# Performance work log

Measured on AMD Instinct MI355X. Metric: run time of the kernel, lower is better.

Reference implementation:

```python
import jax, jax.numpy as jnp
import numpy as np

LEAK_RATE = 0.2
SPECTRAL_RADIUS = 0.9


def setup_inputs() -> dict:
    key = jax.random.key(0)
    k1, k2, k3 = jax.random.split(key, 3)
    B, T, D, U = 32, 1024, 256, 1024
    # glorot-uniform-like init
    lim_w = np.sqrt(6.0 / (U + U)).astype(np.float32)
    lim_in = np.sqrt(6.0 / (D + U)).astype(np.float32)
    W = jax.random.uniform(k1, (U, U), jnp.float32, -lim_w, lim_w)
    # rescale reservoir to target spectral radius (done once at build, like the tf layer)
    eig = np.linalg.eigvals(np.asarray(W))
    W = W * (SPECTRAL_RADIUS / np.max(np.abs(eig)).astype(np.float32))
    W_in = jax.random.uniform(k2, (D, U), jnp.float32, -lim_in, lim_in)
    x = jax.random.normal(k3, (B, T, D), jnp.float32)
    return {"x": x, "W": W, "W_in": W_in}


def reference(x, W, W_in):
    # x: [B, T, D] -> outputs [B, T, U]
    B = x.shape[0]
    U = W.shape[0]
    # precompute input projection for all timesteps: [B, T, U]
    xin = jnp.einsum('btd,du->btu', x, W_in)
    xin_t = jnp.swapaxes(xin, 0, 1)  # [T, B, U]

    def step(h, u_t):
        h_new = (1.0 - LEAK_RATE) * h + LEAK_RATE * jnp.tanh(u_t + h @ W)
        return h_new, h_new

    h0 = jnp.zeros((B, U), x.dtype)
    _, ys = jax.lax.scan(step, h0, xin_t)  # ys: [T, B, U]
    return jnp.swapaxes(ys, 0, 1)  # [B, T, U]
```

## Files before the change

kernel.cpp:

```cpp
#include <hip/hip_runtime.h>
#include <stdint.h>


#define T_   1024
#define D_   256
#define U_   1024
#define NTHR 512
#define HROW 1040
#define BAIL (1u << 20)

typedef _Float16     f16x8 __attribute__((ext_vector_type(8)));
typedef float        f32x4 __attribute__((ext_vector_type(4)));
typedef unsigned int u32x4 __attribute__((ext_vector_type(4)));

#if defined(__has_builtin) && __has_builtin(__builtin_amdgcn_rcpf)
__device__ __forceinline__ float rcp_fast(float v) { return __builtin_amdgcn_rcpf(v); }
#else
__device__ __forceinline__ float rcp_fast(float v) { return 1.f / v; }
#endif

__device__ __forceinline__ float tanh_fast(float v) {
    float e = __expf(2.f * v);
    return 1.f - 2.f * rcp_fast(e + 1.f);
}

__device__ __forceinline__ unsigned f2u16(_Float16 v) {
    return (unsigned)__builtin_bit_cast(unsigned short, v);
}

__device__ __forceinline__ void lds_barrier() {
    asm volatile("s_waitcnt lgkmcnt(0)" ::: "memory");
    __builtin_amdgcn_sched_barrier(0);
    __builtin_amdgcn_s_barrier();
}

__device__ __forceinline__ void lds_fence() {
    asm volatile("s_waitcnt lgkmcnt(0)" ::: "memory");
    __builtin_amdgcn_sched_barrier(0);
}

__global__ __launch_bounds__(NTHR, 2) void k_recur(const float* __restrict__ x,
                                                   const float* __restrict__ W,
                                                   const float* __restrict__ win,
                                                   float* __restrict__ out,
                                                   u32x4* __restrict__ hc) {
    __shared__ short hl16[4 * HROW];
    __shared__ f32x4 part4[256];
    unsigned int* hl32 = (unsigned int*)hl16;

    const int tid  = threadIdx.x;
    const int dom  = blockIdx.x & 7;
    const int wg   = blockIdx.x >> 3;
    const int c0   = wg * 32;
    const int b0   = dom * 4;
    const int lane = tid & 63;
    const int wv   = tid >> 6;
    const int l15  = lane & 15;
    const int lg   = lane >> 4;

    f16x8 bw[5][2];
#pragma unroll
    for (int kt = 0; kt < 4; ++kt)
#pragma unroll
        for (int ct = 0; ct < 2; ++ct)
#pragma unroll
            for (int j = 0; j < 8; ++j)
                bw[kt][ct][j] =
                    (_Float16)W[(size_t)(wv * 128 + kt * 32 + lg * 8 + j) * U_ + c0 + ct * 16 + l15];
#pragma unroll
    for (int ct = 0; ct < 2; ++ct)
#pragma unroll
        for (int j = 0; j < 8; ++j)
            bw[4][ct][j] =
                (_Float16)win[(size_t)(wv * 32 + lg * 8 + j) * U_ + c0 + ct * 16 + l15];

    for (int i = tid; i < 2 * HROW; i += NTHR) hl32[i] = 0;
    __syncthreads();

    const int ab = (l15 & 3) * HROW + lg * 8;
    const float* xg = &x[((size_t)(b0 + (l15 & 3)) * T_) * D_ + wv * 32 + lg * 8];

    float4 xa = *(const float4*)xg;
    float4 xc = *(const float4*)(xg + 4);
    xg += D_;

    float hs0 = 0.f, hs1 = 0.f, hs2 = 0.f, hs3 = 0.f;

    for (int t = 0; t < T_; ++t) {
        u32x4 va, vb;
        if (t > 0) {
            const u32x4* pp = hc + (size_t)((t & 1) * 8192 + dom * 1024 + 2 * tid);
            unsigned spin = 0;
            int ok;
            for (;;) {
                asm volatile(
                    "global_load_dwordx4 %0, %2, off sc1\n\t"
                    "global_load_dwordx4 %1, %2, off offset:16 sc1\n\t"
                    "s_waitcnt vmcnt(0)"
                    : "=&v"(va), "=&v"(vb)
                    : "v"(pp) : "memory");
                unsigned tg = (unsigned)t;
                ok = ((va[0] & 0xffffu) == tg) & ((va[1] & 0xffffu) == tg) &
                     ((va[2] & 0xffffu) == tg) & ((va[3] & 0xffffu) == tg) &
                     ((vb[0] & 0xffffu) == tg) & ((vb[1] & 0xffffu) == tg) &
                     ((vb[2] & 0xffffu) == tg) & ((vb[3] & 0xffffu) == tg);
                if (__all(ok) || ++spin > BAIL) break;
                __builtin_amdgcn_s_sleep(1);
            }
#pragma unroll
            for (int b = 0; b < 4; ++b)
                hl32[b * (HROW / 2) + tid] = (va[b] >> 16) | (vb[b] & 0xffff0000u);
        }

        f16x8 xf;
        xf[0] = (_Float16)xa.x; xf[1] = (_Float16)xa.y;
        xf[2] = (_Float16)xa.z; xf[3] = (_Float16)xa.w;
        xf[4] = (_Float16)xc.x; xf[5] = (_Float16)xc.y;
        xf[6] = (_Float16)xc.z; xf[7] = (_Float16)xc.w;

        lds_fence();

        if (t + 1 < T_) {
            xa = *(const float4*)xg;
            xc = *(const float4*)(xg + 4);
            xg += D_;
        }

        f32x4 acc0 = {0.f, 0.f, 0.f, 0.f}, acc1 = {0.f, 0.f, 0.f, 0.f};
#pragma unroll
        for (int kt = 0; kt < 4; ++kt) {
            f16x8 av = *reinterpret_cast<const f16x8*>(&hl16[ab + wv * 128 + kt * 32]);
            acc0 = __builtin_amdgcn_mfma_f32_16x16x32_f16(av, bw[kt][0], acc0, 0, 0, 0);
            acc1 = __builtin_amdgcn_mfma_f32_16x16x32_f16(av, bw[kt][1], acc1, 0, 0, 0);
        }
        acc0 = __builtin_amdgcn_mfma_f32_16x16x32_f16(xf, bw[4][0], acc0, 0, 0, 0);
        acc1 = __builtin_amdgcn_mfma_f32_16x16x32_f16(xf, bw[4][1], acc1, 0, 0, 0);

        if (lane < 16) {
            part4[wv * 32 + l15]      = acc0;
            part4[wv * 32 + 16 + l15] = acc1;
        }
        lds_barrier();

        if (tid < 32) {
            f32x4 s = part4[tid];
#pragma unroll
            for (int w2 = 1; w2 < 8; ++w2) s += part4[w2 * 32 + tid];
            float h0 = 0.8f * hs0 + 0.2f * tanh_fast(s[0]);
            float h1 = 0.8f * hs1 + 0.2f * tanh_fast(s[1]);
            float h2 = 0.8f * hs2 + 0.2f * tanh_fast(s[2]);
            float h3 = 0.8f * hs3 + 0.2f * tanh_fast(s[3]);
            hs0 = h0; hs1 = h1; hs2 = h2; hs3 = h3;
            unsigned tg = (unsigned)(t + 1) & 0xffffu;
            unsigned p0 = (f2u16((_Float16)h0) << 16) | tg;
            unsigned p1 = (f2u16((_Float16)h1) << 16) | tg;
            unsigned p2 = (f2u16((_Float16)h2) << 16) | tg;
            unsigned p3 = (f2u16((_Float16)h3) << 16) | tg;
            unsigned long long q0 = (unsigned long long)p0 | ((unsigned long long)p1 << 32);
            unsigned long long q1 = (unsigned long long)p2 | ((unsigned long long)p3 << 32);
            unsigned long long* dst = (unsigned long long*)
                (hc + (size_t)((((t + 1) & 1) * 8192) + dom * 1024 + c0 + tid));
            __hip_atomic_store(&dst[0], q0, __ATOMIC_RELAXED, __HIP_MEMORY_SCOPE_AGENT);
            __hip_atomic_store(&dst[1], q1, __ATOMIC_RELAXED, __HIP_MEMORY_SCOPE_AGENT);
            size_t ob = ((size_t)b0 * T_ + t) * U_ + c0 + tid;
            out[ob]                       = h0;
            out[ob + (size_t)T_ * U_]     = h1;
            out[ob + (size_t)2 * T_ * U_] = h2;
            out[ob + (size_t)3 * T_ * U_] = h3;
        }
        lds_barrier();
    }
}

extern "C" void kernel_launch(void* const* d_in, const int* in_sizes, int n_in,
                              void* d_out, int out_size, void* d_ws, size_t ws_size,
                              hipStream_t stream) {
    const float* x   = (const float*)d_in[0];
    const float* W   = (const float*)d_in[1];
    const float* win = (const float*)d_in[2];
    float* out = (float*)d_out;

    u32x4* hc = (u32x4*)d_ws;
    if (ws_size < 2 * 8 * 1024 * 16) return;

    hipMemsetAsync(d_ws, 0, 2 * 8 * 1024 * 16, stream);
    k_recur<<<dim3(256), dim3(NTHR), 0, stream>>>(x, W, win, out, hc);
}
```

Baseline: 1.429 ms.

## Double-buffer partial sums and spread the epilogue across all waves

The partial-sum LDS buffer is double-buffered by timestep parity, which lets the second block barrier per step go away. The reduction, tanh, publish and output store are now spread over 16 lanes in each of the 8 waves, each handling one (column, batch) element, instead of 32 threads in one wave handling four batches each. This shortens the serial critical path of each recurrent step. The cost is a larger LDS footprint and more, smaller scattered global stores per step.

```diff
diff --git a/kernel.cpp b/kernel.cpp
--- a/kernel.cpp
+++ b/kernel.cpp
@@ -45,8 +45,10 @@
                                                    float* __restrict__ out,
                                                    u32x4* __restrict__ hc) {
     __shared__ short hl16[4 * HROW];
-    __shared__ f32x4 part4[256];
-    unsigned int* hl32 = (unsigned int*)hl16;
+    __shared__ f32x4 part4[2][256];
+    unsigned int* hl32  = (unsigned int*)hl16;
+    float*        partf = (float*)part4;
+    unsigned int* hc32  = (unsigned int*)hc;
 
     const int tid  = threadIdx.x;
     const int dom  = blockIdx.x & 7;
@@ -84,7 +86,9 @@
     float4 xc = *(const float4*)(xg + 4);
     xg += D_;
 
-    float hs0 = 0.f, hs1 = 0.f, hs2 = 0.f, hs3 = 0.f;
+    const int fcol = wv * 4 + (l15 >> 2);
+    const int fbat = lane & 3;
+    float hs = 0.f;
 
     for (int t = 0; t < T_; ++t) {
         u32x4 va, vb;
@@ -137,38 +141,24 @@
         acc1 = __builtin_amdgcn_mfma_f32_16x16x32_f16(xf, bw[4][1], acc1, 0, 0, 0);
 
         if (lane < 16) {
-            part4[wv * 32 + l15]      = acc0;
-            part4[wv * 32 + 16 + l15] = acc1;
+            part4[t & 1][wv * 32 + l15]      = acc0;
+            part4[t & 1][wv * 32 + 16 + l15] = acc1;
         }
         lds_barrier();
 
-        if (tid < 32) {
-            f32x4 s = part4[tid];
+        if (lane < 16) {
+            float s = 0.f;
 #pragma unroll
-            for (int w2 = 1; w2 < 8; ++w2) s += part4[w2 * 32 + tid];
-            float h0 = 0.8f * hs0 + 0.2f * tanh_fast(s[0]);
-            float h1 = 0.8f * hs1 + 0.2f * tanh_fast(s[1]);
-            float h2 = 0.8f * hs2 + 0.2f * tanh_fast(s[2]);
-            float h3 = 0.8f * hs3 + 0.2f * tanh_fast(s[3]);
-            hs0 = h0; hs1 = h1; hs2 = h2; hs3 = h3;
-            unsigned tg = (unsigned)(t + 1) & 0xffffu;
-            unsigned p0 = (f2u16((_Float16)h0) << 16) | tg;
-            unsigned p1 = (f2u16((_Float16)h1) << 16) | tg;
-            unsigned p2 = (f2u16((_Float16)h2) << 16) | tg;
-            unsigned p3 = (f2u16((_Float16)h3) << 16) | tg;
-            unsigned long long q0 = (unsigned long long)p0 | ((unsigned long long)p1 << 32);
-            unsigned long long q1 = (unsigned long long)p2 | ((unsigned long long)p3 << 32);
-            unsigned long long* dst = (unsigned long long*)
-                (hc + (size_t)((((t + 1) & 1) * 8192) + dom * 1024 + c0 + tid));
-            __hip_atomic_store(&dst[0], q0, __ATOMIC_RELAXED, __HIP_MEMORY_SCOPE_AGENT);
-            __hip_atomic_store(&dst[1], q1, __ATOMIC_RELAXED, __HIP_MEMORY_SCOPE_AGENT);
-            size_t ob = ((size_t)b0 * T_ + t) * U_ + c0 + tid;
-            out[ob]                       = h0;
-            out[ob + (size_t)T_ * U_]     = h1;
-            out[ob + (size_t)2 * T_ * U_] = h2;
-            out[ob + (size_t)3 * T_ * U_] = h3;
+            for (int w2 = 0; w2 < 8; ++w2)
+                s += partf[(t & 1) * 1024 + (w2 * 32 + fcol) * 4 + fbat];
+            float hn = 0.8f * hs + 0.2f * tanh_fast(s);
+            hs = hn;
+            unsigned pk = (f2u16((_Float16)hn) << 16) | ((unsigned)(t + 1) & 0xffffu);
+            __hip_atomic_store(
+                &hc32[(size_t)(((t + 1) & 1) * 32768 + dom * 4096 + (c0 + fcol) * 4 + fbat)],
+                pk, __ATOMIC_RELAXED, __HIP_MEMORY_SCOPE_AGENT);
+            out[((size_t)(b0 + fbat) * T_ + t) * U_ + c0 + fcol] = hn;
         }
-        lds_barrier();
     }
 }
 
```

After: 1.757 ms. +23.0%, slower.
